# Kernel optimization log

Measured on AMD Instinct MI355X. Metric: run time of the kernel, lower is better.

## Reference

```python
import jax, jax.numpy as jnp
import numpy as np

B, T, U = 8, 256, 64
ENC_DIM, DEC_DIM, JOINT_DIM, VOCAB = 512, 512, 640, 1024


def setup_inputs() -> dict:
    key = jax.random.key(0)
    k1, k2, k3, k4, k5 = jax.random.split(key, 5)
    s_enc = 1.0 / np.sqrt(ENC_DIM)
    s_dec = 1.0 / np.sqrt(DEC_DIM)
    s_joint = 1.0 / np.sqrt(JOINT_DIM)
    return {
        "enc_out": jax.random.normal(k1, (B, T, ENC_DIM), dtype=jnp.float32),
        "pred_out": jax.random.normal(k2, (B, U, DEC_DIM), dtype=jnp.float32),
        # nn.Linear weights stored as [out, in], applied as x @ W.T
        "W_enc": jax.random.uniform(k3, (JOINT_DIM, ENC_DIM), jnp.float32, -s_enc, s_enc),
        "W_pred": jax.random.uniform(k4, (JOINT_DIM, DEC_DIM), jnp.float32, -s_dec, s_dec),
        "W_out": jax.random.uniform(k5, (VOCAB, JOINT_DIM), jnp.float32, -s_joint, s_joint),
    }


def reference(enc_out, pred_out, W_enc, W_pred, W_out):
    # project: [B,T,J] and [B,U,J]
    enc_p = jnp.einsum("bte,je->btj", enc_out, W_enc)
    pred_p = jnp.einsum("bud,jd->buj", pred_out, W_pred)
    # broadcast add -> [B,T,U,J], SiLU, then output GEMM -> [B,T,U,V]
    joint = enc_p[:, :, None, :] + pred_p[:, None, :, :]
    joint = joint * jax.nn.sigmoid(joint)  # SiLU
    out = jnp.einsum("btuj,vj->btuv", joint, W_out)
    return out
```

## Files before the change

kernel.cpp:

```cpp
#include <hip/hip_runtime.h>

typedef unsigned short u16;
typedef __attribute__((ext_vector_type(8))) short short8;
typedef __attribute__((ext_vector_type(8))) unsigned short ushort8v;
typedef __attribute__((ext_vector_type(4))) float f32x4;

#define B_ 8
#define T_ 256
#define U_ 64
#define E_ 512
#define J_ 640
#define V_ 1024
#define NT 20

__device__ __forceinline__ u16 f2bf(float f) {
  unsigned int u = __float_as_uint(f);
  u += 0x7fffu + ((u >> 16) & 1u);
  return (u16)(u >> 16);
}

__device__ __forceinline__ void gload16(const void* g, void* l) {
  __builtin_amdgcn_global_load_lds((const __attribute__((address_space(1))) void*)g,
                                   (__attribute__((address_space(3))) void*)l,
                                   16, 0, 0);
}

__global__ __launch_bounds__(256) void cast5_k(const float4* __restrict__ s0,
                                               const float4* __restrict__ s1,
                                               const float4* __restrict__ s2,
                                               const float4* __restrict__ s3,
                                               const float4* __restrict__ s4,
                                               ushort4* __restrict__ dst) {
  int i = blockIdx.x * 256 + threadIdx.x;
  const int st = gridDim.x * 256;
  for (; i < 655360; i += st) {
    const float4* s; int off;
    if (i < 262144)      { s = s0; off = 0; }
    else if (i < 327680) { s = s1; off = 262144; }
    else if (i < 409600) { s = s2; off = 327680; }
    else if (i < 491520) { s = s3; off = 409600; }
    else                 { s = s4; off = 491520; }
    float4 v = s[i - off];
    ushort4 o;
    o.x = f2bf(v.x); o.y = f2bf(v.y); o.z = f2bf(v.z); o.w = f2bf(v.w);
    dst[i] = o;
  }
}

__global__ __launch_bounds__(256) void proj_k(const u16* __restrict__ X,
                                              const u16* __restrict__ W,
                                              float* __restrict__ C) {
  __shared__ __align__(16) u16 As[128 * 32];
  __shared__ __align__(16) u16 Bs[128 * 32];
  const int tid = threadIdx.x;
  const int w = tid >> 6, lane = tid & 63;
  const int wr = w >> 1, wc = w & 1;
  const int m0 = blockIdx.x * 128, n0 = blockIdx.y * 128;
  const int lr = lane & 15, lk = lane >> 4;
  const int r4 = tid >> 2, kq = tid & 3;

  f32x4 acc[4][4] = {};

  for (int ks = 0; ks < E_ / 32; ++ks) {
    const int k0 = ks * 32;
    gload16(X + (size_t)(m0 + r4) * E_ + k0 + kq * 8, (char*)As + w * 1024);
    gload16(X + (size_t)(m0 + 64 + r4) * E_ + k0 + kq * 8, (char*)As + 4096 + w * 1024);
    gload16(W + (size_t)(n0 + r4) * E_ + k0 + kq * 8, (char*)Bs + w * 1024);
    gload16(W + (size_t)(n0 + 64 + r4) * E_ + k0 + kq * 8, (char*)Bs + 4096 + w * 1024);
    __syncthreads();
    short8 a[4], bb[4];
#pragma unroll
    for (int m = 0; m < 4; ++m)
      a[m] = *(const short8*)&As[(wr * 64 + m * 16 + lr) * 32 + lk * 8];
#pragma unroll
    for (int n = 0; n < 4; ++n)
      bb[n] = *(const short8*)&Bs[(wc * 64 + n * 16 + lr) * 32 + lk * 8];
#pragma unroll
    for (int m = 0; m < 4; ++m)
#pragma unroll
      for (int n = 0; n < 4; ++n)
        acc[m][n] = __builtin_amdgcn_mfma_f32_16x16x32_bf16(a[m], bb[n], acc[m][n], 0, 0, 0);
    __syncthreads();
  }

#pragma unroll
  for (int m = 0; m < 4; ++m) {
    const int row = m0 + wr * 64 + m * 16 + lk * 4;
#pragma unroll
    for (int n = 0; n < 4; ++n) {
      const int col = n0 + wc * 64 + n * 16 + lr;
#pragma unroll
      for (int i = 0; i < 4; ++i)
        C[(size_t)(row + i) * J_ + col] = acc[m][n][i];
    }
  }
}

__global__ __launch_bounds__(256) void pack_k(const u16* __restrict__ Wo,
                                              u16* __restrict__ pk) {
  const int u = blockIdx.x * 256 + threadIdx.x;
  const int l = u & 63;
  int r = u >> 6;
  const int nq = r & 3;  r >>= 2;
  const int ks = r % 20;
  const int vt = r / 20;
  const int v = vt * 64 + nq * 16 + (l & 15);
  const int k = ks * 32 + (l >> 4) * 8;
  *(short8*)(pk + (size_t)u * 8) = *(const short8*)(Wo + (size_t)v * J_ + k);
}

__global__ __launch_bounds__(512, 2) void fused2_k(const float* __restrict__ ep,
                                                   const float* __restrict__ pp,
                                                   const u16* __restrict__ pk,
                                                   float* __restrict__ out) {
  __shared__ __align__(16) u16 Alds[64 * 640];
  const int tid = threadIdx.x;
  const int w = tid >> 6, lane = tid & 63;
  const int lr = lane & 15, lk = lane >> 4;
  const int bt = blockIdx.x;
  const int b = bt >> 8;
  const size_t m0 = (size_t)bt * 64;

  const u16* bp0 = pk + (size_t)(w * 2) * 40960 + lane * 8;
  const u16* bp1 = bp0 + 40960;

  short8 BE[8], BO[8], aE[4], aO[4];

#define BL(bF, ks)                                                             \
  do {                                                                         \
    _Pragma("unroll")                                                          \
    for (int nq = 0; nq < 4; ++nq) {                                           \
      bF[nq]     = *(const short8*)(bp0 + (ks) * 2048 + nq * 512);             \
      bF[4 + nq] = *(const short8*)(bp1 + (ks) * 2048 + nq * 512);             \
    }                                                                          \
  } while (0)

  BL(BE, 0);

  const float* eprow = ep + (size_t)bt * J_;
  const float* pbase = pp + (size_t)b * 64 * J_;
#pragma unroll
  for (int it = 0; it < 10; ++it) {
    const int unit = tid + it * 512;
    const int row = unit / 80;
    const int c = unit - row * 80;
    union { float4 v[2]; float f[8]; } Ee, Pp;
    Ee.v[0] = *(const float4*)(eprow + c * 8);
    Ee.v[1] = *(const float4*)(eprow + c * 8 + 4);
    Pp.v[0] = *(const float4*)(pbase + (size_t)row * J_ + c * 8);
    Pp.v[1] = *(const float4*)(pbase + (size_t)row * J_ + c * 8 + 4);
    union { ushort8v v; u16 s[8]; } R;
#pragma unroll
    for (int j = 0; j < 8; ++j) {
      float x = Ee.f[j] + Pp.f[j];
      R.s[j] = f2bf(x * __builtin_amdgcn_rcpf(1.0f + __expf(-x)));
    }
    *(ushort8v*)&Alds[row * 640 + ((c ^ (row & 7)) << 3)] = R.v;
  }
  __syncthreads();

  const int rx = lr & 7;
  int arow[4];
#pragma unroll
  for (int mq = 0; mq < 4; ++mq) arow[mq] = (mq * 16 + lr) * 640;

#define AR(aF, ks)                                                             \
  do {                                                                         \
    _Pragma("unroll")                                                          \
    for (int mq = 0; mq < 4; ++mq)                                             \
      aF[mq] = *(const short8*)&Alds[arow[mq] + ((((ks) * 4 + lk) ^ rx) << 3)];\
  } while (0)

#define MM(aF, bF)                                                             \
  do {                                                                         \
    __builtin_amdgcn_s_setprio(1);                                             \
    _Pragma("unroll")                                                          \
    for (int mq = 0; mq < 4; ++mq)                                             \
      _Pragma("unroll")                                                        \
      for (int nq = 0; nq < 8; ++nq)                                           \
        acc[mq][nq] = __builtin_amdgcn_mfma_f32_16x16x32_bf16(bF[nq], aF[mq],  \
                                                              acc[mq][nq], 0, 0, 0); \
    __builtin_amdgcn_s_setprio(0);                                             \
  } while (0)

  f32x4 acc[4][8] = {};
  AR(aE, 0);

#pragma unroll 1
  for (int ks = 0; ks < NT; ks += 2) {
    BL(BO, ks + 1);
    AR(aO, ks + 1);
    MM(aE, BE);
    __builtin_amdgcn_sched_barrier(0);
    if (ks + 2 < NT) { BL(BE, ks + 2); AR(aE, ks + 2); }
    MM(aO, BO);
    __builtin_amdgcn_sched_barrier(0);
  }

  const int col0 = w * 128;
#pragma unroll
  for (int mq = 0; mq < 4; ++mq) {
    const size_t row = m0 + mq * 16 + lr;
#pragma unroll
    for (int nq = 0; nq < 8; ++nq) {
      const int col = col0 + nq * 16 + lk * 4;
      *(float4*)&out[row * V_ + col] = *(float4*)&acc[mq][nq];
    }
  }
#undef AR
#undef BL
#undef MM
}

extern "C" void kernel_launch(void* const* d_in, const int* in_sizes, int n_in,
                              void* d_out, int out_size, void* d_ws, size_t ws_size,
                              hipStream_t stream) {
  const float* enc = (const float*)d_in[0];
  const float* pred = (const float*)d_in[1];
  const float* We = (const float*)d_in[2];
  const float* Wp = (const float*)d_in[3];
  const float* Wo = (const float*)d_in[4];
  float* out = (float*)d_out;

  char* ws = (char*)d_ws;
  u16* enc_bf = (u16*)ws;
  u16* pred_bf = (u16*)(ws + 2097152);
  u16* We_bf = (u16*)(ws + 2621440);
  u16* Wp_bf = (u16*)(ws + 3276800);
  u16* Wo_bf = (u16*)(ws + 3932160);
  float* ep = (float*)(ws + 5242880);
  float* pp = (float*)(ws + 10485760);
  u16* Wo_pk = (u16*)(ws + 11796480);

  cast5_k<<<2048, 256, 0, stream>>>((const float4*)enc, (const float4*)pred,
                                    (const float4*)We, (const float4*)Wp,
                                    (const float4*)Wo, (ushort4*)ws);

  proj_k<<<dim3(16, 5), 256, 0, stream>>>(enc_bf, We_bf, ep);
  proj_k<<<dim3(4, 5), 256, 0, stream>>>(pred_bf, Wp_bf, pp);
  pack_k<<<320, 256, 0, stream>>>(Wo_bf, Wo_pk);

  fused2_k<<<2048, 512, 0, stream>>>(ep, pp, Wo_pk, out);
}
```

Measured before the change: 250.8 us.

## Split output tile across 16 waves per block instead of 8

Measured after the change: 249.7 us. About the same (-0.4%).

```diff
diff --git a/kernel.cpp b/kernel.cpp
--- a/kernel.cpp
+++ b/kernel.cpp
@@ -109,10 +109,10 @@
   *(short8*)(pk + (size_t)u * 8) = *(const short8*)(Wo + (size_t)v * J_ + k);
 }
 
-__global__ __launch_bounds__(512, 2) void fused2_k(const float* __restrict__ ep,
-                                                   const float* __restrict__ pp,
-                                                   const u16* __restrict__ pk,
-                                                   float* __restrict__ out) {
+__global__ __launch_bounds__(1024, 1) void fused3_k(const float* __restrict__ ep,
+                                                    const float* __restrict__ pp,
+                                                    const u16* __restrict__ pk,
+                                                    float* __restrict__ out) {
   __shared__ __align__(16) u16 Alds[64 * 640];
   const int tid = threadIdx.x;
   const int w = tid >> 6, lane = tid & 63;
@@ -121,18 +121,15 @@
   const int b = bt >> 8;
   const size_t m0 = (size_t)bt * 64;
 
-  const u16* bp0 = pk + (size_t)(w * 2) * 40960 + lane * 8;
-  const u16* bp1 = bp0 + 40960;
-
-  short8 BE[8], BO[8], aE[4], aO[4];
+  const u16* bp = pk + (size_t)w * 40960 + lane * 8;
+
+  short8 BE[4], BO[4], a[4];
 
 #define BL(bF, ks)                                                             \
   do {                                                                         \
     _Pragma("unroll")                                                          \
-    for (int nq = 0; nq < 4; ++nq) {                                           \
-      bF[nq]     = *(const short8*)(bp0 + (ks) * 2048 + nq * 512);             \
-      bF[4 + nq] = *(const short8*)(bp1 + (ks) * 2048 + nq * 512);             \
-    }                                                                          \
+    for (int nq = 0; nq < 4; ++nq)                                             \
+      bF[nq] = *(const short8*)(bp + (ks) * 2048 + nq * 512);                  \
   } while (0)
 
   BL(BE, 0);
@@ -140,8 +137,8 @@
   const float* eprow = ep + (size_t)bt * J_;
   const float* pbase = pp + (size_t)b * 64 * J_;
 #pragma unroll
-  for (int it = 0; it < 10; ++it) {
-    const int unit = tid + it * 512;
+  for (int it = 0; it < 5; ++it) {
+    const int unit = tid + it * 1024;
     const int row = unit / 80;
     const int c = unit - row * 80;
     union { float4 v[2]; float f[8]; } Ee, Pp;
@@ -160,50 +157,47 @@
   __syncthreads();
 
   const int rx = lr & 7;
-  int arow[4];
-#pragma unroll
-  for (int mq = 0; mq < 4; ++mq) arow[mq] = (mq * 16 + lr) * 640;
-
-#define AR(aF, ks)                                                             \
+
+#define AR(ks)                                                                 \
   do {                                                                         \
     _Pragma("unroll")                                                          \
     for (int mq = 0; mq < 4; ++mq)                                             \
-      aF[mq] = *(const short8*)&Alds[arow[mq] + ((((ks) * 4 + lk) ^ rx) << 3)];\
+      a[mq] = *(const short8*)&Alds[(mq * 16 + lr) * 640 +                     \
+                                    ((((ks) * 4 + lk) ^ rx) << 3)];            \
   } while (0)
 
-#define MM(aF, bF)                                                             \
+#define MM(bF)                                                                 \
   do {                                                                         \
     __builtin_amdgcn_s_setprio(1);                                             \
     _Pragma("unroll")                                                          \
     for (int mq = 0; mq < 4; ++mq)                                             \
       _Pragma("unroll")                                                        \
-      for (int nq = 0; nq < 8; ++nq)                                           \
-        acc[mq][nq] = __builtin_amdgcn_mfma_f32_16x16x32_bf16(bF[nq], aF[mq],  \
+      for (int nq = 0; nq < 4; ++nq)                                           \
+        acc[mq][nq] = __builtin_amdgcn_mfma_f32_16x16x32_bf16(bF[nq], a[mq],   \
                                                               acc[mq][nq], 0, 0, 0); \
     __builtin_amdgcn_s_setprio(0);                                             \
   } while (0)
 
-  f32x4 acc[4][8] = {};
-  AR(aE, 0);
+  f32x4 acc[4][4] = {};
 
 #pragma unroll 1
   for (int ks = 0; ks < NT; ks += 2) {
+    AR(ks);
     BL(BO, ks + 1);
-    AR(aO, ks + 1);
-    MM(aE, BE);
+    MM(BE);
     __builtin_amdgcn_sched_barrier(0);
-    if (ks + 2 < NT) { BL(BE, ks + 2); AR(aE, ks + 2); }
-    MM(aO, BO);
+    AR(ks + 1);
+    if (ks + 2 < NT) BL(BE, ks + 2);
+    MM(BO);
     __builtin_amdgcn_sched_barrier(0);
   }
 
-  const int col0 = w * 128;
 #pragma unroll
   for (int mq = 0; mq < 4; ++mq) {
     const size_t row = m0 + mq * 16 + lr;
 #pragma unroll
-    for (int nq = 0; nq < 8; ++nq) {
-      const int col = col0 + nq * 16 + lk * 4;
+    for (int nq = 0; nq < 4; ++nq) {
+      const int col = w * 64 + nq * 16 + lk * 4;
       *(float4*)&out[row * V_ + col] = *(float4*)&acc[mq][nq];
     }
   }
@@ -240,5 +234,5 @@
   proj_k<<<dim3(4, 5), 256, 0, stream>>>(pred_bf, Wp_bf, pp);
   pack_k<<<320, 256, 0, stream>>>(Wo_bf, Wo_pk);
 
-  fused2_k<<<2048, 512, 0, stream>>>(ep, pp, Wo_pk, out);
-}
+  fused3_k<<<2048, 1024, 0, stream>>>(ep, pp, Wo_pk, out);
+}
```
